# Performance work log

Measured on AMD Instinct MI355X. Metric: run time of the kernel, lower is better.

## Reference

```python
import jax, jax.numpy as jnp
import numpy as np

D_MODEL = 1024
NUM_HEADS = 16
D_K = D_MODEL // NUM_HEADS


def setup_inputs() -> dict:
    key = jax.random.key(0)
    ks = jax.random.split(key, 11)
    s = 1.0 / np.sqrt(D_MODEL)
    return {
        "Q": jax.random.normal(ks[0], (2, 2048, D_MODEL), jnp.float32),
        "K": jax.random.normal(ks[1], (2, 2048, D_MODEL), jnp.float32),
        "V": jax.random.normal(ks[2], (2, 2048, D_MODEL), jnp.float32),
        "W_Q": jax.random.uniform(ks[3], (D_MODEL, D_MODEL), jnp.float32, -s, s),
        "b_Q": jax.random.uniform(ks[4], (D_MODEL,), jnp.float32, -s, s),
        "W_K": jax.random.uniform(ks[5], (D_K, D_MODEL), jnp.float32, -s, s),
        "b_K": jax.random.uniform(ks[6], (D_K,), jnp.float32, -s, s),
        "W_V": jax.random.uniform(ks[7], (D_K, D_MODEL), jnp.float32, -s, s),
        "b_V": jax.random.uniform(ks[8], (D_K,), jnp.float32, -s, s),
        "W_O": jax.random.uniform(ks[9], (D_MODEL, D_MODEL), jnp.float32, -s, s),
        "b_O": jax.random.uniform(ks[10], (D_MODEL,), jnp.float32, -s, s),
    }


def reference(Q, K, V, W_Q, b_Q, W_K, b_K, W_V, b_V, W_O, b_O):
    B, S, _ = Q.shape
    # Q projection -> [B, H, S, d_k]
    q = (Q @ W_Q.T + b_Q).reshape(B, S, NUM_HEADS, D_K).transpose(0, 2, 1, 3)
    # shared single-head K/V -> [B, S, d_k] (broadcast across heads)
    k = K @ W_K.T + b_K
    v = V @ W_V.T + b_V
    scale = 1.0 / jnp.sqrt(jnp.asarray(D_K, q.dtype))
    scores = jnp.einsum('bhqd,bkd->bhqk', q, k) * scale  # [B,H,S,S]
    attn = jax.nn.softmax(scores, axis=-1)
    out = jnp.einsum('bhqk,bkd->bhqd', attn, v)  # [B,H,S,d_k]
    out = out.transpose(0, 2, 1, 3).reshape(B, S, D_MODEL)
    return out @ W_O.T + b_O
```

## Files before the change

kernel.cpp:

```cpp
#include <hip/hip_runtime.h>
#include <hip/hip_bf16.h>
#include <math.h>

#define D_MODEL 1024
#define NUM_HEADS 16
#define DK 64
#define BATCH 2
#define SEQ 2048
#define MROWS (BATCH * SEQ)

#define QSCALE (0.125f * 1.4426950408889634f)

typedef __attribute__((ext_vector_type(8))) short bf16x8;
typedef __attribute__((ext_vector_type(4))) float f32x4;

static __device__ __forceinline__ short f2bf(float f) {
    __hip_bfloat16 h = __float2bfloat16(f);
    union { __hip_bfloat16 h; short s; } c; c.h = h; return c.s;
}

static __device__ __forceinline__ unsigned pkbf2(float a, float b) {
    __hip_bfloat162 h = __float22bfloat162_rn(make_float2(a, b));
    union { __hip_bfloat162 h; unsigned u; } c; c.h = h; return c.u;
}

static __device__ __forceinline__ void gload16(const void* g, void* l) {
    __builtin_amdgcn_global_load_lds(
        (const __attribute__((address_space(1))) unsigned int*)g,
        (__attribute__((address_space(3))) unsigned int*)l, 16, 0, 0);
}

__global__ __launch_bounds__(256) void cvt6(
    const float* __restrict__ q, const float* __restrict__ k,
    const float* __restrict__ v, const float* __restrict__ wq,
    const float* __restrict__ wo, const float* __restrict__ wk,
    const float* __restrict__ wv,
    short* __restrict__ qo, short* __restrict__ ko, short* __restrict__ vo,
    short* __restrict__ wqo, short* __restrict__ woo, short* __restrict__ wko,
    short* __restrict__ wvo)
{
    const int NB = (MROWS * D_MODEL) / 8;
    const int NW = (D_MODEL * D_MODEL) / 8;
    const int NS = (DK * D_MODEL) / 8;
    const int total = 3 * NB + 2 * NW + 2 * NS;
    for (int g = blockIdx.x * 256 + threadIdx.x; g < total; g += gridDim.x * 256) {
        const float* s; short* d; int x = g;
        if (x < NB)            { s = q;  d = qo;  }
        else if ((x -= NB) < NB) { s = k;  d = ko;  }
        else if ((x -= NB) < NB) { s = v;  d = vo;  }
        else if ((x -= NB) < NW) { s = wq; d = wqo; }
        else if ((x -= NW) < NW) { s = wo; d = woo; }
        else if ((x -= NW) < NS) { s = wk; d = wko; }
        else                     { x -= NS; s = wv; d = wvo; }
        float4 a = ((const float4*)s)[x * 2];
        float4 b = ((const float4*)s)[x * 2 + 1];
        uint4 hv;
        hv.x = pkbf2(a.x, a.y); hv.y = pkbf2(a.z, a.w);
        hv.z = pkbf2(b.x, b.y); hv.w = pkbf2(b.z, b.w);
        ((uint4*)d)[x] = hv;
    }
}

template<int MODE, int BM, int BN>
__global__ __launch_bounds__(256) void gemm97(
    const short* __restrict__ A, const short* __restrict__ W,
    const float* __restrict__ bias, void* __restrict__ Cp,
    const short* __restrict__ A2, const short* __restrict__ W2,
    const float* __restrict__ bias2, void* __restrict__ Cp2,
    int M, int N, int K, float outmult)
{
    constexpr int MI = BM / 32;
    constexpr int NI = BN / 32;
    constexpr int ACH = BM / 32;
    constexpr int WCH = BN / 32;
    __shared__ short As[BM * 64];
    __shared__ short Ws[BN * 64];

    int sel = 0;
    if (MODE == 2) {
        sel = blockIdx.y;
        if (sel) { A = A2; W = W2; bias = bias2; Cp = Cp2; }
    }
    const int bm = blockIdx.x * BM;
    const int bn = (MODE == 2) ? 0 : blockIdx.y * BN;
    const int tid = threadIdx.x;
    const int l = tid & 63, w = tid >> 6;
    const int lr = l & 15, lg = l >> 4;
    const int wm = (w >> 1) * (BM / 2), wn = (w & 1) * (BN / 2);

    f32x4 acc[MI][NI];
    #pragma unroll
    for (int mi = 0; mi < MI; mi++)
        #pragma unroll
        for (int ni = 0; ni < NI; ni++)
            acc[mi][ni] = (f32x4){0.f, 0.f, 0.f, 0.f};

    const int srow = l >> 3;
    const int scol = (l & 7) * 8;

    for (int k0 = 0; k0 < K; k0 += 64) {
        __syncthreads();
        #pragma unroll
        for (int i = 0; i < ACH; i++) {
            int c = w * ACH + i;
            gload16(A + (size_t)(bm + 8 * c + srow) * K + k0 + scol, As + c * 512);
        }
        #pragma unroll
        for (int i = 0; i < WCH; i++) {
            int c = w * WCH + i;
            gload16(W + (size_t)(bn + 8 * c + srow) * K + k0 + scol, Ws + c * 512);
        }
        __syncthreads();
        #pragma unroll
        for (int ks = 0; ks < 2; ks++) {
            bf16x8 af[MI], bf[NI];
            #pragma unroll
            for (int mi = 0; mi < MI; mi++)
                af[mi] = *(const bf16x8*)&As[(wm + mi * 16 + lr) * 64 + ks * 32 + 8 * lg];
            #pragma unroll
            for (int ni = 0; ni < NI; ni++)
                bf[ni] = *(const bf16x8*)&Ws[(wn + ni * 16 + lr) * 64 + ks * 32 + 8 * lg];
            #pragma unroll
            for (int mi = 0; mi < MI; mi++)
                #pragma unroll
                for (int ni = 0; ni < NI; ni++)
                    acc[mi][ni] = __builtin_amdgcn_mfma_f32_16x16x32_bf16(
                        af[mi], bf[ni], acc[mi][ni], 0, 0, 0);
        }
    }

    #pragma unroll
    for (int ni = 0; ni < NI; ni++) {
        int col = bn + wn + ni * 16 + lr;
        float bv = bias[col];
        #pragma unroll
        for (int mi = 0; mi < MI; mi++) {
            #pragma unroll
            for (int r = 0; r < 4; r++) {
                int row = bm + wm + mi * 16 + lg * 4 + r;
                float val = (acc[mi][ni][r] + bv) * outmult;
                if (MODE == 0) {
                    ((short*)Cp)[(size_t)row * N + col] = f2bf(val);
                } else if (MODE == 1) {
                    ((float*)Cp)[(size_t)row * N + col] = val;
                } else {
                    if (sel == 0) {
                        ((short*)Cp)[(size_t)row * DK + col] = f2bf(val);
                    } else {
                        int bi = row >> 11, si = row & (SEQ - 1);
                        int s6 = si & 63;
                        int sperm = (si & ~63) | (s6 & 32) |
                                    (((s6 >> 3) & 1) << 4) | (((s6 >> 2) & 1) << 3) |
                                    (((s6 >> 4) & 1) << 2) | (s6 & 3);
                        ((short*)Cp)[((size_t)bi * DK + col) * SEQ + sperm] = f2bf(val);
                    }
                }
            }
        }
    }
}

__global__ __launch_bounds__(512, 4) void mqa_attn_lds(
    const short* __restrict__ qb, const short* __restrict__ kb,
    const short* __restrict__ vt, short* __restrict__ ob)
{
    __shared__ char KsB[2][64 * 128];
    __shared__ char VsB[2][64 * 128];
    __shared__ float ML[128];
    const int b = blockIdx.z;
    const int tid = threadIdx.x;
    const int l = tid & 63, w = tid >> 6;
    const int h2 = w >> 2, qg = (w >> 1) & 1, kh = w & 1;
    const int hd = blockIdx.y * 2 + h2;
    const int lr = l & 15, lg = l >> 4;
    const int q0 = blockIdx.x * 64 + qg * 32;

    bf16x8 qf[2][2];
    #pragma unroll
    for (int qt = 0; qt < 2; qt++)
        #pragma unroll
        for (int kk = 0; kk < 2; kk++)
            qf[qt][kk] = *(const bf16x8*)(
                qb + (size_t)(b * SEQ + q0 + qt * 16 + lr) * D_MODEL + hd * DK + kk * 32 + 8 * lg);

    const int srow = tid >> 3;
    const int scol = (((tid & 7) * 16) ^ ((srow & 7) << 4)) >> 1;

    f32x4 o[4][2];
    #pragma unroll
    for (int dt = 0; dt < 4; dt++)
        #pragma unroll
        for (int qt = 0; qt < 2; qt++)
            o[dt][qt] = (f32x4){0.f, 0.f, 0.f, 0.f};
    float l_l[2] = {0.f, 0.f};

    gload16(kb + (size_t)(b * SEQ + 0 + srow) * DK + scol, KsB[0] + w * 64 * 16);
    gload16(vt + (size_t)(b * DK + srow) * SEQ + 0 + scol, VsB[0] + w * 64 * 16);

    for (int t = 0; t < SEQ / 64; t++) {
        const int cur = t & 1;
        const int kt = t * 64;
        __syncthreads();
        if (t + 1 < SEQ / 64) {
            const int ktn = kt + 64;
            gload16(kb + (size_t)(b * SEQ + ktn + srow) * DK + scol,
                    KsB[cur ^ 1] + w * 64 * 16);
            gload16(vt + (size_t)(b * DK + srow) * SEQ + ktn + scol,
                    VsB[cur ^ 1] + w * 64 * 16);
        }
        const char* Kc = KsB[cur];
        const char* Vc = VsB[cur];

        f32x4 s[2][2];
        #pragma unroll
        for (int qt = 0; qt < 2; qt++)
            #pragma unroll
            for (int j = 0; j < 2; j++) s[qt][j] = (f32x4){0.f, 0.f, 0.f, 0.f};
        #pragma unroll
        for (int kk = 0; kk < 2; kk++) {
            bf16x8 kf[2];
            #pragma unroll
            for (int j = 0; j < 2; j++) {
                int row = kh * 32 + j * 16 + lr;
                kf[j] = *(const bf16x8*)(Kc + row * 128 + ((kk * 64 + 16 * lg) ^ ((row & 7) << 4)));
            }
            __builtin_amdgcn_s_setprio(1);
            #pragma unroll
            for (int qt = 0; qt < 2; qt++)
                #pragma unroll
                for (int j = 0; j < 2; j++)
                    s[qt][j] = __builtin_amdgcn_mfma_f32_16x16x32_bf16(
                        kf[j], qf[qt][kk], s[qt][j], 0, 0, 0);
            __builtin_amdgcn_s_setprio(0);
        }

        bf16x8 vf[4];
        #pragma unroll
        for (int dt = 0; dt < 4; dt++) {
            int row = dt * 16 + lr;
            vf[dt] = *(const bf16x8*)(Vc + row * 128 + ((kh * 64 + 16 * lg) ^ ((row & 7) << 4)));
        }

        union { unsigned u[4]; bf16x8 v; } pku[2];
        #pragma unroll
        for (int qt = 0; qt < 2; qt++) {
            float p[2][4];
            float rs = 0.f;
            #pragma unroll
            for (int j = 0; j < 2; j++) {
                p[j][0] = __builtin_amdgcn_exp2f(s[qt][j][0]);
                p[j][1] = __builtin_amdgcn_exp2f(s[qt][j][1]);
                p[j][2] = __builtin_amdgcn_exp2f(s[qt][j][2]);
                p[j][3] = __builtin_amdgcn_exp2f(s[qt][j][3]);
                rs += (p[j][0] + p[j][1]) + (p[j][2] + p[j][3]);
            }
            l_l[qt] += rs;
            pku[qt].u[0] = pkbf2(p[0][0], p[0][1]);
            pku[qt].u[1] = pkbf2(p[0][2], p[0][3]);
            pku[qt].u[2] = pkbf2(p[1][0], p[1][1]);
            pku[qt].u[3] = pkbf2(p[1][2], p[1][3]);
        }

        __builtin_amdgcn_s_setprio(1);
        #pragma unroll
        for (int dt = 0; dt < 4; dt++)
            #pragma unroll
            for (int qt = 0; qt < 2; qt++)
                o[dt][qt] = __builtin_amdgcn_mfma_f32_16x16x32_bf16(
                    vf[dt], pku[qt].v, o[dt][qt], 0, 0, 0);
        __builtin_amdgcn_s_setprio(0);
    }

    float lw[2];
    #pragma unroll
    for (int qt = 0; qt < 2; qt++) {
        float x = l_l[qt];
        x += __shfl_xor(x, 16);
        x += __shfl_xor(x, 32);
        lw[qt] = x;
    }
    __syncthreads();
    float* OS = h2 ? (float*)VsB : (float*)KsB;
    if (kh == 1) {
        #pragma unroll
        for (int dt = 0; dt < 4; dt++)
            #pragma unroll
            for (int qt = 0; qt < 2; qt++)
                #pragma unroll
                for (int r = 0; r < 4; r++)
                    OS[(dt * 8 + qt * 4 + r) * 128 + qg * 64 + l] = o[dt][qt][r];
        if (l < 16) {
            ML[((h2 * 2 + qg) * 2 + 0) * 16 + l] = lw[0];
            ML[((h2 * 2 + qg) * 2 + 1) * 16 + l] = lw[1];
        }
    }
    __syncthreads();
    if (kh == 0) {
        #pragma unroll
        for (int qt = 0; qt < 2; qt++) {
            float lt = lw[qt] + ML[((h2 * 2 + qg) * 2 + qt) * 16 + lr];
            float inv = 1.0f / lt;
            size_t grow = (size_t)(b * SEQ + q0 + qt * 16 + lr);
            #pragma unroll
            for (int dt = 0; dt < 4; dt++) {
                float v0 = o[dt][qt][0] + OS[(dt * 8 + qt * 4 + 0) * 128 + qg * 64 + l];
                float v1 = o[dt][qt][1] + OS[(dt * 8 + qt * 4 + 1) * 128 + qg * 64 + l];
                float v2 = o[dt][qt][2] + OS[(dt * 8 + qt * 4 + 2) * 128 + qg * 64 + l];
                float v3 = o[dt][qt][3] + OS[(dt * 8 + qt * 4 + 3) * 128 + qg * 64 + l];
                uint2 pk;
                pk.x = pkbf2(v0 * inv, v1 * inv);
                pk.y = pkbf2(v2 * inv, v3 * inv);
                *(uint2*)(ob + grow * D_MODEL + hd * DK + dt * 16 + lg * 4) = pk;
            }
        }
    }
}

extern "C" void kernel_launch(void* const* d_in, const int* in_sizes, int n_in,
                              void* d_out, int out_size, void* d_ws, size_t ws_size,
                              hipStream_t stream) {
    const float* Q   = (const float*)d_in[0];
    const float* K   = (const float*)d_in[1];
    const float* V   = (const float*)d_in[2];
    const float* W_Q = (const float*)d_in[3];
    const float* b_Q = (const float*)d_in[4];
    const float* W_K = (const float*)d_in[5];
    const float* b_K = (const float*)d_in[6];
    const float* W_V = (const float*)d_in[7];
    const float* b_V = (const float*)d_in[8];
    const float* W_O = (const float*)d_in[9];
    const float* b_O = (const float*)d_in[10];
    float* out = (float*)d_out;

    short* Qb  = (short*)d_ws;
    short* Kb  = Qb  + (size_t)MROWS * D_MODEL;
    short* Vb  = Kb  + (size_t)MROWS * D_MODEL;
    short* WQb = Vb  + (size_t)MROWS * D_MODEL;
    short* WKb = WQb + (size_t)D_MODEL * D_MODEL;
    short* WVb = WKb + (size_t)DK * D_MODEL;
    short* WOb = WVb + (size_t)DK * D_MODEL;
    short* qb  = WOb + (size_t)D_MODEL * D_MODEL;
    short* kb  = qb  + (size_t)MROWS * D_MODEL;
    short* vt  = kb  + (size_t)MROWS * DK;
    short* aws = vt  + (size_t)MROWS * DK;

    cvt6<<<2048, 256, 0, stream>>>(Q, K, V, W_Q, W_O, W_K, W_V,
                                   Qb, Kb, Vb, WQb, WOb, WKb, WVb);

    gemm97<0, 64, 128><<<dim3(MROWS / 64, D_MODEL / 128), 256, 0, stream>>>(
        Qb, WQb, b_Q, qb, nullptr, nullptr, nullptr, nullptr,
        MROWS, D_MODEL, D_MODEL, QSCALE);
    gemm97<2, 64, 64><<<dim3(MROWS / 64, 2), 256, 0, stream>>>(
        Kb, WKb, b_K, kb, Vb, WVb, b_V, vt, MROWS, DK, D_MODEL, 1.0f);
    mqa_attn_lds<<<dim3(SEQ / 64, NUM_HEADS / 2, BATCH), 512, 0, stream>>>(
        qb, kb, vt, aws);
    gemm97<1, 64, 128><<<dim3(MROWS / 64, D_MODEL / 128), 256, 0, stream>>>(
        aws, WOb, b_O, out, nullptr, nullptr, nullptr, nullptr,
        MROWS, D_MODEL, D_MODEL, 1.0f);
}
```

Measured before the change: 116.2 us.

## Process four heads per attention block to share K/V tiles across more waves

The attention kernel now uses 1024-thread blocks covering four heads instead of two, halving the grid's y dimension. Each shared K/V tile loaded into LDS is reused by twice as many waves, and the load work is split so the first 8 waves load K and the rest load V. The epilogue reduction is done in two phases because LDS scratch only holds two heads at once, which adds extra barriers. Risks are larger blocks hurting occupancy and scheduling flexibility, and launch_bounds(1024,8) putting pressure on registers.

```diff
diff --git a/kernel.cpp b/kernel.cpp
--- a/kernel.cpp
+++ b/kernel.cpp
@@ -160,18 +160,18 @@
     }
 }
 
-__global__ __launch_bounds__(512, 4) void mqa_attn_lds(
+__global__ __launch_bounds__(1024, 8) void mqa_attn_lds(
     const short* __restrict__ qb, const short* __restrict__ kb,
     const short* __restrict__ vt, short* __restrict__ ob)
 {
     __shared__ char KsB[2][64 * 128];
     __shared__ char VsB[2][64 * 128];
-    __shared__ float ML[128];
+    __shared__ float ML[256];
     const int b = blockIdx.z;
     const int tid = threadIdx.x;
     const int l = tid & 63, w = tid >> 6;
     const int h2 = w >> 2, qg = (w >> 1) & 1, kh = w & 1;
-    const int hd = blockIdx.y * 2 + h2;
+    const int hd = blockIdx.y * 4 + h2;
     const int lr = l & 15, lg = l >> 4;
     const int q0 = blockIdx.x * 64 + qg * 32;
 
@@ -183,8 +183,10 @@
             qf[qt][kk] = *(const bf16x8*)(
                 qb + (size_t)(b * SEQ + q0 + qt * 16 + lr) * D_MODEL + hd * DK + kk * 32 + 8 * lg);
 
-    const int srow = tid >> 3;
-    const int scol = (((tid & 7) * 16) ^ ((srow & 7) << 4)) >> 1;
+    const int sc = (w & 7) * 64 + l;
+    const int srow = sc >> 3;
+    const int scol = (((sc & 7) * 16) ^ ((srow & 7) << 4)) >> 1;
+    const bool doK = (w < 8);
 
     f32x4 o[4][2];
     #pragma unroll
@@ -194,8 +196,8 @@
             o[dt][qt] = (f32x4){0.f, 0.f, 0.f, 0.f};
     float l_l[2] = {0.f, 0.f};
 
-    gload16(kb + (size_t)(b * SEQ + 0 + srow) * DK + scol, KsB[0] + w * 64 * 16);
-    gload16(vt + (size_t)(b * DK + srow) * SEQ + 0 + scol, VsB[0] + w * 64 * 16);
+    if (doK) gload16(kb + (size_t)(b * SEQ + 0 + srow) * DK + scol, KsB[0] + sc * 16);
+    else     gload16(vt + (size_t)(b * DK + srow) * SEQ + 0 + scol, VsB[0] + sc * 16);
 
     for (int t = 0; t < SEQ / 64; t++) {
         const int cur = t & 1;
@@ -203,10 +205,10 @@
         __syncthreads();
         if (t + 1 < SEQ / 64) {
             const int ktn = kt + 64;
-            gload16(kb + (size_t)(b * SEQ + ktn + srow) * DK + scol,
-                    KsB[cur ^ 1] + w * 64 * 16);
-            gload16(vt + (size_t)(b * DK + srow) * SEQ + ktn + scol,
-                    VsB[cur ^ 1] + w * 64 * 16);
+            if (doK) gload16(kb + (size_t)(b * SEQ + ktn + srow) * DK + scol,
+                             KsB[cur ^ 1] + sc * 16);
+            else     gload16(vt + (size_t)(b * DK + srow) * SEQ + ktn + scol,
+                             VsB[cur ^ 1] + sc * 16);
         }
         const char* Kc = KsB[cur];
         const char* Vc = VsB[cur];
@@ -280,39 +282,43 @@
         lw[qt] = x;
     }
     __syncthreads();
-    float* OS = h2 ? (float*)VsB : (float*)KsB;
-    if (kh == 1) {
-        #pragma unroll
-        for (int dt = 0; dt < 4; dt++)
-            #pragma unroll
-            for (int qt = 0; qt < 2; qt++)
+    float* OS = (h2 & 1) ? (float*)VsB : (float*)KsB;
+    if (kh == 1 && l < 16) {
+        ML[((h2 * 2 + qg) * 2 + 0) * 16 + l] = lw[0];
+        ML[((h2 * 2 + qg) * 2 + 1) * 16 + l] = lw[1];
+    }
+    #pragma unroll
+    for (int ph = 0; ph < 2; ph++) {
+        if ((h2 >> 1) == ph && kh == 1) {
+            #pragma unroll
+            for (int dt = 0; dt < 4; dt++)
                 #pragma unroll
-                for (int r = 0; r < 4; r++)
-                    OS[(dt * 8 + qt * 4 + r) * 128 + qg * 64 + l] = o[dt][qt][r];
-        if (l < 16) {
-            ML[((h2 * 2 + qg) * 2 + 0) * 16 + l] = lw[0];
-            ML[((h2 * 2 + qg) * 2 + 1) * 16 + l] = lw[1];
-        }
-    }
-    __syncthreads();
-    if (kh == 0) {
-        #pragma unroll
-        for (int qt = 0; qt < 2; qt++) {
-            float lt = lw[qt] + ML[((h2 * 2 + qg) * 2 + qt) * 16 + lr];
-            float inv = 1.0f / lt;
-            size_t grow = (size_t)(b * SEQ + q0 + qt * 16 + lr);
-            #pragma unroll
-            for (int dt = 0; dt < 4; dt++) {
-                float v0 = o[dt][qt][0] + OS[(dt * 8 + qt * 4 + 0) * 128 + qg * 64 + l];
-                float v1 = o[dt][qt][1] + OS[(dt * 8 + qt * 4 + 1) * 128 + qg * 64 + l];
-                float v2 = o[dt][qt][2] + OS[(dt * 8 + qt * 4 + 2) * 128 + qg * 64 + l];
-                float v3 = o[dt][qt][3] + OS[(dt * 8 + qt * 4 + 3) * 128 + qg * 64 + l];
-                uint2 pk;
-                pk.x = pkbf2(v0 * inv, v1 * inv);
-                pk.y = pkbf2(v2 * inv, v3 * inv);
-                *(uint2*)(ob + grow * D_MODEL + hd * DK + dt * 16 + lg * 4) = pk;
+                for (int qt = 0; qt < 2; qt++)
+                    #pragma unroll
+                    for (int r = 0; r < 4; r++)
+                        OS[(dt * 8 + qt * 4 + r) * 128 + qg * 64 + l] = o[dt][qt][r];
+        }
+        __syncthreads();
+        if ((h2 >> 1) == ph && kh == 0) {
+            #pragma unroll
+            for (int qt = 0; qt < 2; qt++) {
+                float lt = lw[qt] + ML[((h2 * 2 + qg) * 2 + qt) * 16 + lr];
+                float inv = 1.0f / lt;
+                size_t grow = (size_t)(b * SEQ + q0 + qt * 16 + lr);
+                #pragma unroll
+                for (int dt = 0; dt < 4; dt++) {
+                    float v0 = o[dt][qt][0] + OS[(dt * 8 + qt * 4 + 0) * 128 + qg * 64 + l];
+                    float v1 = o[dt][qt][1] + OS[(dt * 8 + qt * 4 + 1) * 128 + qg * 64 + l];
+                    float v2 = o[dt][qt][2] + OS[(dt * 8 + qt * 4 + 2) * 128 + qg * 64 + l];
+                    float v3 = o[dt][qt][3] + OS[(dt * 8 + qt * 4 + 3) * 128 + qg * 64 + l];
+                    uint2 pk;
+                    pk.x = pkbf2(v0 * inv, v1 * inv);
+                    pk.y = pkbf2(v2 * inv, v3 * inv);
+                    *(uint2*)(ob + grow * D_MODEL + hd * DK + dt * 16 + lg * 4) = pk;
+                }
             }
         }
+        __syncthreads();
     }
 }
 
@@ -352,7 +358,7 @@
         MROWS, D_MODEL, D_MODEL, QSCALE);
     gemm97<2, 64, 64><<<dim3(MROWS / 64, 2), 256, 0, stream>>>(
         Kb, WKb, b_K, kb, Vb, WVb, b_V, vt, MROWS, DK, D_MODEL, 1.0f);
-    mqa_attn_lds<<<dim3(SEQ / 64, NUM_HEADS / 2, BATCH), 512, 0, stream>>>(
+    mqa_attn_lds<<<dim3(SEQ / 64, NUM_HEADS / 4, BATCH), 1024, 0, stream>>>(
         qb, kb, vt, aws);
     gemm97<1, 64, 128><<<dim3(MROWS / 64, D_MODEL / 128), 256, 0, stream>>>(
         aws, WOb, b_O, out, nullptr, nullptr, nullptr, nullptr,
```

Measured after the change: 340.5 us. 193% more time.
